# Performance work log

Measured on AMD Instinct MI355X. Metric: run time of the kernel, lower is better.

## Reference

```python
import jax, jax.numpy as jnp
import numpy as np

B, L, D, H = 2, 1024, 1024, 16
HEAD = D // H
BUCKETS = 256
MAX_REL = 512
ATT_SPAN = BUCKETS          # pos_ebd_size = position_buckets when buckets > 0
SCALE_FACTOR = 3            # 1 (content) + 1 (c2p) + 1 (p2c)


def _log_bucket(rel, bucket_size, max_position):
    """make_log_bucket_position: signed log-bucketed relative positions."""
    sign = jnp.sign(rel).astype(jnp.float32)
    mid = bucket_size // 2
    abs_pos = jnp.where((rel < mid) & (rel > -mid), mid - 1, jnp.abs(rel)).astype(jnp.float32)
    log_pos = jnp.ceil(jnp.log(abs_pos / mid) / np.float32(np.log((max_position - 1) / mid)) * (mid - 1)) + mid
    bucket = jnp.where(abs_pos <= mid, rel.astype(jnp.float32), log_pos * sign)
    return bucket.astype(jnp.int32)


def build_relative_position(q_len, k_len):
    rel = jnp.arange(q_len, dtype=jnp.int32)[:, None] - jnp.arange(k_len, dtype=jnp.int32)[None, :]
    return _log_bucket(rel, BUCKETS, MAX_REL)  # [q_len, k_len]


def setup_inputs() -> dict:
    key = jax.random.key(0)
    ks = jax.random.split(key, 6)
    w = 0.02  # typical init scale, keeps softmax well-conditioned
    return {
        "hidden_states": jax.random.normal(ks[0], (B, L, D), jnp.float32),
        "attention_mask": jnp.ones((B, L), jnp.int32),
        "rel_embeddings": jax.random.normal(ks[1], (2 * ATT_SPAN, D), jnp.float32) * w,
        "Wq": jax.random.normal(ks[2], (D, D), jnp.float32) * w,
        "bq": jnp.zeros((D,), jnp.float32),
        "Wk": jax.random.normal(ks[3], (D, D), jnp.float32) * w,
        "bk": jnp.zeros((D,), jnp.float32),
        "Wv": jax.random.normal(ks[4], (D, D), jnp.float32) * w,
        "bv": jnp.zeros((D,), jnp.float32),
    }


def reference(hidden_states, attention_mask, rel_embeddings, Wq, bq, Wk, bk, Wv, bv):
    Bn, Ln, Dn = hidden_states.shape

    def proj(x, W, b):  # Linear with bias, torch convention y = x W^T + b
        return x @ W.T + b

    def to_heads(x):  # [.., L, D] -> [.., H, L, HEAD]
        return x.reshape(*x.shape[:-1], H, HEAD).swapaxes(-3, -2)

    q = to_heads(proj(hidden_states, Wq, bq))  # [B,H,L,d]
    k = to_heads(proj(hidden_states, Wk, bk))
    v = to_heads(proj(hidden_states, Wv, bv))

    scale = jnp.sqrt(jnp.float32(HEAD * SCALE_FACTOR))
    scores = jnp.einsum('bhqd,bhkd->bhqk', q, k) / scale

    # disentangled relative-position bias (share_att_key=True -> reuse Wq/Wk)
    rel = build_relative_position(Ln, Ln)                     # [L,L] log-bucketed
    pos_k = proj(rel_embeddings, Wk, bk).reshape(2 * ATT_SPAN, H, HEAD)
    pos_q = proj(rel_embeddings, Wq, bq).reshape(2 * ATT_SPAN, H, HEAD)

    # c2p: Q . posK, gathered at (rel + span)
    c2p_att = jnp.einsum('bhqd,phd->bhqp', q, pos_k)          # [B,H,L,2S]
    c2p_idx = jnp.clip(rel + ATT_SPAN, 0, 2 * ATT_SPAN - 1)   # [L,L]
    c2p = jnp.take_along_axis(c2p_att, jnp.broadcast_to(c2p_idx[None, None], (Bn, H, Ln, Ln)), axis=-1)

    # p2c: K . posQ gathered at (-rel + span), then transposed to [q,k]
    p2c_att = jnp.einsum('bhkd,phd->bhkp', k, pos_q)          # [B,H,L,2S]
    p2c_idx = jnp.clip(-rel + ATT_SPAN, 0, 2 * ATT_SPAN - 1)
    p2c = jnp.take_along_axis(p2c_att, jnp.broadcast_to(p2c_idx[None, None], (Bn, H, Ln, Ln)), axis=-1)
    p2c = jnp.swapaxes(p2c, -1, -2)

    scores = scores + (c2p + p2c) / scale

    bias = jnp.where(attention_mask[:, None, None, :] > 0, 0.0, -1e9).astype(scores.dtype)
    probs = jax.nn.softmax(scores + bias, axis=-1)
    ctx = jnp.einsum('bhqk,bhkd->bhqd', probs, v)
    return ctx.swapaxes(1, 2).reshape(Bn, Ln, Dn)
```

## Files before the change

kernel.cpp:

```cpp
#include <hip/hip_runtime.h>


typedef short s8v __attribute__((ext_vector_type(8)));
typedef short s4v __attribute__((ext_vector_type(4)));
typedef float f32x4 __attribute__((ext_vector_type(4)));
typedef float f4v __attribute__((ext_vector_type(4)));

#define QK_SCALE 0.26864243f

__device__ __forceinline__ unsigned short f2bf(float f) {
  unsigned u = __builtin_bit_cast(unsigned, f);
  u += 0x7fffu + ((u >> 16) & 1u);
  return (unsigned short)(u >> 16);
}
__device__ __forceinline__ float bf2f(unsigned short h) {
  unsigned u = ((unsigned)h) << 16;
  return __builtin_bit_cast(float, u);
}

__device__ __forceinline__ void gload_lds16(const void* g, void* l) {
  __builtin_amdgcn_global_load_lds(
      (const __attribute__((address_space(1))) void*)g,
      (__attribute__((address_space(3))) void*)l, 16, 0, 0);
}

__global__ __launch_bounds__(256) void prep_kernel(
    const float* __restrict__ hidden, const float* __restrict__ rel,
    const float* __restrict__ Wq, const float* __restrict__ Wk,
    const float* __restrict__ Wv, const int* __restrict__ mask,
    short* __restrict__ Abf, short* __restrict__ Wbf,
    float* __restrict__ mbias, short* __restrict__ Tt) {
  int idx = blockIdx.x * 256 + threadIdx.x;
  const int NCONV = 1441792;
  if (idx < NCONV) {
    const float* src; short* dst; int off;
    if (idx < 524288) { src = hidden; dst = Abf; off = idx; }
    else if (idx < 655360) { src = rel; dst = Abf + 2048 * 1024; off = idx - 524288; }
    else {
      int j = idx - 655360;
      int w = j / 262144; off = j - w * 262144;
      src = (w == 0) ? Wq : (w == 1) ? Wk : Wv;
      dst = Wbf + w * 1048576;
    }
    f4v v = ((const f4v*)src)[off];
    s4v o;
    o[0] = (short)f2bf(v[0]); o[1] = (short)f2bf(v[1]);
    o[2] = (short)f2bf(v[2]); o[3] = (short)f2bf(v[3]);
    ((s4v*)dst)[off] = o;
  } else {
    int j = idx - NCONV;
    if (j < 2047) {
      int r = j - 1023;
      float fr = (float)r;
      float sign = (r > 0) ? 1.f : ((r < 0) ? -1.f : 0.f);
      float abs_pos = (r < 128 && r > -128) ? 127.f : fabsf(fr);
      const float logc = 1.3843393245589053f;
      float log_pos = ceilf(logf(abs_pos * (1.f / 128.f)) / logc * 127.f) + 128.f;
      float bucket = (abs_pos <= 128.f) ? fr : log_pos * sign;
      int bi = (int)bucket + 256;
      bi = bi < 0 ? 0 : (bi > 511 ? 511 : bi);
      Tt[j] = (short)bi;
    } else if (j < 4095) {
      int m = j - 2047;
      mbias[m] = (mask[m] > 0) ? 0.f : -1e9f;
    }
  }
}

__global__ __launch_bounds__(256) void gemm_qkv(
    const short* __restrict__ Abf, const short* __restrict__ Wbf,
    const float* __restrict__ bq, const float* __restrict__ bk,
    const float* __restrict__ bv,
    short* __restrict__ Qc, short* __restrict__ Kc, short* __restrict__ Vc) {
  __shared__ short As[128 * 64];
  __shared__ short Bs[128 * 64];
  int tid = threadIdx.x;
  int wid = tid >> 6, lane = tid & 63;
  int lr = lane & 15, lg = lane >> 4;
  int wr = wid >> 1, wc = wid & 1;
  int z = blockIdx.z;
  int brow = blockIdx.y * 128;
  if (z == 2 && brow >= 2048) return;
  const short* W = Wbf + z * 1048576;
  const float* bias = (z == 0) ? bq : (z == 1) ? bk : bv;
  short* C = (z == 0) ? Qc : (z == 1) ? Kc : Vc;
  float scale = (z == 2) ? 1.f : QK_SCALE;
  int bcol = blockIdx.x * 128;

  f32x4 acc[4][4];
  for (int i = 0; i < 4; i++)
    for (int j = 0; j < 4; j++) acc[i][j] = (f32x4){0.f, 0.f, 0.f, 0.f};

  for (int k0 = 0; k0 < 1024; k0 += 64) {
    for (int i = 0; i < 4; i++) {
      int n = i * 256 + wid * 64 + lane;
      const short* gA = Abf + (size_t)(brow + (n >> 3)) * 1024 + k0 + (n & 7) * 8;
      gload_lds16(gA, &As[(i * 256 + wid * 64) * 8]);
      const short* gB = W + (size_t)(bcol + (n >> 3)) * 1024 + k0 + (n & 7) * 8;
      gload_lds16(gB, &Bs[(i * 256 + wid * 64) * 8]);
    }
    __syncthreads();
    for (int ks = 0; ks < 2; ks++) {
      s8v af[4], bfv[4];
      for (int mi = 0; mi < 4; mi++)
        af[mi] = *(const s8v*)&As[(wr * 64 + mi * 16 + lr) * 64 + ks * 32 + lg * 8];
      for (int ni = 0; ni < 4; ni++)
        bfv[ni] = *(const s8v*)&Bs[(wc * 64 + ni * 16 + lr) * 64 + ks * 32 + lg * 8];
      for (int mi = 0; mi < 4; mi++)
        for (int ni = 0; ni < 4; ni++)
          acc[mi][ni] = __builtin_amdgcn_mfma_f32_16x16x32_bf16(
              af[mi], bfv[ni], acc[mi][ni], 0, 0, 0);
    }
    __syncthreads();
  }
  for (int mi = 0; mi < 4; mi++)
    for (int ni = 0; ni < 4; ni++) {
      int col = bcol + wc * 64 + ni * 16 + lr;
      float bb = bias[col];
      for (int r = 0; r < 4; r++) {
        int row = brow + wr * 64 + mi * 16 + lg * 4 + r;
        float v = (acc[mi][ni][r] + bb) * scale;
        C[(size_t)row * 1024 + col] = (short)f2bf(v);
      }
    }
}

__global__ __launch_bounds__(256) void pos_gemm(
    const short* __restrict__ Qc, const short* __restrict__ Kc,
    const float* __restrict__ mbias,
    short* __restrict__ c2p, short* __restrict__ p2c) {
  __shared__ short As[128 * 64];
  __shared__ short Bs[128 * 64];
  int tid = threadIdx.x;
  int wid = tid >> 6, lane = tid & 63;
  int lr = lane & 15, lg = lane >> 4;
  int wr = wid >> 1, wc = wid & 1;
  int zz = blockIdx.z;
  int which = zz >> 5;
  int bh = zz & 31;
  int b = bh >> 4, h = bh & 15;
  const short* Arows = (which == 0) ? Qc : Kc;
  const short* Brows = (which == 0) ? Kc : Qc;
  short* Out = (which == 0) ? c2p : p2c;
  int mrow = blockIdx.y * 128;
  int ncol = blockIdx.x * 128;

  for (int i = 0; i < 4; i++) {
    int n = i * 256 + wid * 64 + lane;
    const short* gA = Arows + (size_t)(b * 1024 + mrow + (n >> 3)) * 1024 + h * 64 + (n & 7) * 8;
    gload_lds16(gA, &As[(i * 256 + wid * 64) * 8]);
    const short* gB = Brows + (size_t)(2048 + ncol + (n >> 3)) * 1024 + h * 64 + (n & 7) * 8;
    gload_lds16(gB, &Bs[(i * 256 + wid * 64) * 8]);
  }
  __syncthreads();

  f32x4 acc[4][4];
  for (int i = 0; i < 4; i++)
    for (int j = 0; j < 4; j++) acc[i][j] = (f32x4){0.f, 0.f, 0.f, 0.f};
  for (int ks = 0; ks < 2; ks++) {
    s8v af[4], bfv[4];
    for (int mi = 0; mi < 4; mi++)
      af[mi] = *(const s8v*)&As[(wr * 64 + mi * 16 + lr) * 64 + ks * 32 + lg * 8];
    for (int ni = 0; ni < 4; ni++)
      bfv[ni] = *(const s8v*)&Bs[(wc * 64 + ni * 16 + lr) * 64 + ks * 32 + lg * 8];
    for (int mi = 0; mi < 4; mi++)
      for (int ni = 0; ni < 4; ni++)
        acc[mi][ni] = __builtin_amdgcn_mfma_f32_16x16x32_bf16(
            af[mi], bfv[ni], acc[mi][ni], 0, 0, 0);
  }
  size_t base = (size_t)(b * 16 + h) * 1024;
  for (int mi = 0; mi < 4; mi++)
    for (int ni = 0; ni < 4; ni++)
      for (int r = 0; r < 4; r++) {
        int m = mrow + wr * 64 + mi * 16 + lg * 4 + r;
        int nn = ncol + wc * 64 + ni * 16 + lr;
        float v = acc[mi][ni][r];
        if (which == 1) v += mbias[b * 1024 + m];
        Out[(base + m) * 512 + nn] = (short)f2bf(v);
      }
}

__global__ __launch_bounds__(256) void transpose_v(
    const short* __restrict__ Vc, short* __restrict__ Vt) {
  __shared__ short TL[64 * 72];
  int tid = threadIdx.x;
  int lt = blockIdx.x, h = blockIdx.y, b = blockIdx.z;
  for (int i = 0; i < 2; i++) {
    int n = i * 256 + tid;
    int l = n >> 3, c = n & 7;
    s8v v = *(const s8v*)&Vc[(size_t)(b * 1024 + lt * 64 + l) * 1024 + h * 64 + c * 8];
    *(s8v*)&TL[l * 72 + c * 8] = v;
  }
  __syncthreads();
  for (int i = 0; i < 2; i++) {
    int m = i * 256 + tid;
    int d = m >> 3, c = m & 7;
    s8v o;
    for (int jj = 0; jj < 8; jj++) o[jj] = TL[(c * 8 + jj) * 72 + d];
    *(s8v*)&Vt[((size_t)(b * 16 + h) * 64 + d) * 1024 + lt * 64 + c * 8] = o;
  }
}

template <int NSPLIT>
__global__ __launch_bounds__(256) void attn_kernel(
    const short* __restrict__ Qc, const short* __restrict__ Kc,
    const short* __restrict__ Vt, const short* __restrict__ c2p,
    const short* __restrict__ p2c, const short* __restrict__ Tt,
    float* __restrict__ Opart, float* __restrict__ dpart,
    float* __restrict__ out) {
  const int KSEG = 1024 / NSPLIT;
  const int NT = KSEG / 64;
  const int TLN = 64 + KSEG - 1;
  __shared__ short Kl[2][64 * 64];
  __shared__ short Vl[2][64 * 64];
  __shared__ short Pl[4][16 * 72];
  __shared__ short Tl[TLN + 1];
  int tid = threadIdx.x;
  int wid = tid >> 6, lane = tid & 63;
  int lr = lane & 15, lg = lane >> 4;
  int qt = blockIdx.x, h = blockIdx.y, z = blockIdx.z;
  int b = (NSPLIT == 1) ? z : (z >> 2);
  int ks = (NSPLIT == 1) ? 0 : (z & 3);
  int k0seg = ks * KSEG;
  int q0 = qt * 64, qbase = q0 + wid * 16;
  size_t bh1024 = (size_t)(b * 16 + h) * 1024;

  for (int i = tid; i < TLN; i += 256) Tl[i] = Tt[(q0 - k0seg - (KSEG - 1) + 1023) + i];

  s8v aq[2];
  for (int s_ = 0; s_ < 2; s_++)
    aq[s_] = *(const s8v*)&Qc[(size_t)(b * 1024 + qbase + lr) * 1024 + h * 64 + s_ * 32 + lg * 8];

  f32x4 oacc[4];
  for (int n = 0; n < 4; n++) oacc[n] = (f32x4){0.f, 0.f, 0.f, 0.f};
  float dsum[4] = {0.f, 0.f, 0.f, 0.f};
  __syncthreads();

  auto stage = [&](int t, int buf) {
#pragma unroll
    for (int i = 0; i < 2; i++) {
      int n = i * 256 + tid;
      int row = n >> 3, cswz = n & 7, cb = cswz ^ (row & 7);
      gload_lds16(&Kc[(size_t)(b * 1024 + k0seg + t * 64 + row) * 1024 + h * 64 + cb * 8],
                  &Kl[buf][(i * 256 + wid * 64) * 8]);
      gload_lds16(&Vt[((size_t)(b * 16 + h) * 64 + row) * 1024 + k0seg + t * 64 + cb * 8],
                  &Vl[buf][(i * 256 + wid * 64) * 8]);
    }
  };
  auto gather = [&](int t, unsigned short* cg, unsigned short* pg) {
#pragma unroll
    for (int n = 0; n < 4; n++) {
      int k = k0seg + t * 64 + n * 16 + lr;
      size_t prow = (bh1024 + k) * 512;
      int jb = wid * 16 - t * 64 - lr + (KSEG - 1) - n * 16 + lg * 4;
#pragma unroll
      for (int r = 0; r < 4; r++) {
        int q = qbase + lg * 4 + r;
        int idx = Tl[jb + r];
        cg[n * 4 + r] = (unsigned short)c2p[(bh1024 + q) * 512 + idx];
        pg[n * 4 + r] = (unsigned short)p2c[prow + idx];
      }
    }
  };

  unsigned short c2g[16], p2g[16], c2n[16], p2n[16];
  stage(0, 0);
  gather(0, c2g, p2g);
  __syncthreads();

#pragma unroll
  for (int t = 0; t < NT; ++t) {
    const int cur = t & 1, nxt = cur ^ 1;

    if (t + 1 < NT) {
      stage(t + 1, nxt);
      gather(t + 1, c2n, p2n);
    }

    f32x4 sacc[4];
#pragma unroll
    for (int n = 0; n < 4; n++) sacc[n] = (f32x4){0.f, 0.f, 0.f, 0.f};
#pragma unroll
    for (int s_ = 0; s_ < 2; s_++)
#pragma unroll
      for (int n = 0; n < 4; n++) {
        int row = n * 16 + lr, cb = s_ * 4 + lg, cbs = cb ^ (row & 7);
        s8v bk_ = *(const s8v*)&Kl[cur][row * 64 + cbs * 8];
        sacc[n] = __builtin_amdgcn_mfma_f32_16x16x32_bf16(aq[s_], bk_, sacc[n], 0, 0, 0);
      }

#pragma unroll
    for (int n = 0; n < 4; n++)
#pragma unroll
      for (int r = 0; r < 4; r++) {
        float bias = bf2f(c2g[n * 4 + r]) + bf2f(p2g[n * 4 + r]);
        float p = __expf(sacc[n][r] + bias);
        dsum[r] += p;
        Pl[wid][(lg * 4 + r) * 72 + n * 16 + lr] = (short)f2bf(p);
      }
    asm volatile("s_waitcnt lgkmcnt(0)" ::: "memory");

#pragma unroll
    for (int s_ = 0; s_ < 2; s_++) {
      s8v ap = *(const s8v*)&Pl[wid][lr * 72 + s_ * 32 + lg * 8];
#pragma unroll
      for (int n = 0; n < 4; n++) {
        int row = n * 16 + lr, cb = s_ * 4 + lg, cbs = cb ^ (row & 7);
        s8v bv_ = *(const s8v*)&Vl[cur][row * 64 + cbs * 8];
        oacc[n] = __builtin_amdgcn_mfma_f32_16x16x32_bf16(ap, bv_, oacc[n], 0, 0, 0);
      }
    }

    __syncthreads();

    if (t + 1 < NT) {
#pragma unroll
      for (int i = 0; i < 16; i++) { c2g[i] = c2n[i]; p2g[i] = p2n[i]; }
    }
  }

  for (int m = 1; m < 16; m <<= 1)
    for (int r = 0; r < 4; r++) dsum[r] += __shfl_xor(dsum[r], m, 64);

  if (NSPLIT == 1) {
    for (int n = 0; n < 4; n++)
      for (int r = 0; r < 4; r++) {
        int q = qbase + lg * 4 + r;
        int d = n * 16 + lr;
        out[(size_t)(b * 1024 + q) * 1024 + h * 64 + d] = oacc[n][r] / dsum[r];
      }
  } else {
    size_t po = ((size_t)(z * 16 + h)) * 65536;
    for (int n = 0; n < 4; n++)
      for (int r = 0; r < 4; r++) {
        int q = qbase + lg * 4 + r;
        Opart[po + (size_t)q * 64 + n * 16 + lr] = oacc[n][r];
      }
    if (lr == 0)
      for (int r = 0; r < 4; r++)
        dpart[(z * 16 + h) * 1024 + qbase + lg * 4 + r] = dsum[r];
  }
}

__global__ __launch_bounds__(256) void combine_kernel(
    const float* __restrict__ Opart, const float* __restrict__ dpart,
    float* __restrict__ out) {
  int idx = blockIdx.x * 256 + threadIdx.x;
  int pos = idx * 4;
  int b = pos >> 20;
  int q = (pos >> 10) & 1023;
  int hd = pos & 1023;
  int h = hd >> 6, d = hd & 63;
  f4v s = (f4v){0.f, 0.f, 0.f, 0.f};
  float dn = 0.f;
  for (int ks = 0; ks < 4; ks++) {
    int zh = (b * 4 + ks) * 16 + h;
    s += *(const f4v*)&Opart[(size_t)zh * 65536 + q * 64 + d];
    dn += dpart[zh * 1024 + q];
  }
  f4v r = s / dn;
  *(f4v*)&out[pos] = r;
}

extern "C" void kernel_launch(void* const* d_in, const int* in_sizes, int n_in,
                              void* d_out, int out_size, void* d_ws, size_t ws_size,
                              hipStream_t stream) {
  (void)in_sizes; (void)n_in; (void)out_size;
  const float* hidden = (const float*)d_in[0];
  const int* mask = (const int*)d_in[1];
  const float* rel = (const float*)d_in[2];
  const float* Wq = (const float*)d_in[3];
  const float* bq = (const float*)d_in[4];
  const float* Wk = (const float*)d_in[5];
  const float* bk = (const float*)d_in[6];
  const float* Wv = (const float*)d_in[7];
  const float* bv = (const float*)d_in[8];
  float* out = (float*)d_out;

  char* w = (char*)d_ws;
  short* Abf = (short*)w; w += 2560 * 1024 * 2;
  short* Wbf = (short*)w; w += 3 * 1024 * 1024 * 2;
  short* Qc  = (short*)w; w += 2560 * 1024 * 2;
  short* Kc  = (short*)w; w += 2560 * 1024 * 2;
  short* Vc  = (short*)w; w += 2560 * 1024 * 2;
  short* Vt  = (short*)w; w += 2 * 16 * 64 * 1024 * 2;
  short* c2p = (short*)w; w += (size_t)2 * 16 * 1024 * 512 * 2;
  short* p2c = (short*)w; w += (size_t)2 * 16 * 1024 * 512 * 2;
  short* Tt  = (short*)w; w += 4096;
  float* mbias = (float*)w; w += 8192;
  float* Opart = (float*)w; w += (size_t)8 * 16 * 1024 * 64 * 4;
  float* dpart = (float*)w; w += 8 * 16 * 1024 * 4;
  size_t need = (size_t)(w - (char*)d_ws);

  prep_kernel<<<5648, 256, 0, stream>>>(hidden, rel, Wq, Wk, Wv, mask, Abf, Wbf, mbias, Tt);
  gemm_qkv<<<dim3(8, 20, 3), 256, 0, stream>>>(Abf, Wbf, bq, bk, bv, Qc, Kc, Vc);
  pos_gemm<<<dim3(4, 8, 64), 256, 0, stream>>>(Qc, Kc, mbias, c2p, p2c);
  transpose_v<<<dim3(16, 16, 2), 256, 0, stream>>>(Vc, Vt);
  if (ws_size >= need) {
    attn_kernel<4><<<dim3(16, 16, 8), 256, 0, stream>>>(Qc, Kc, Vt, c2p, p2c, Tt,
                                                        Opart, dpart, out);
    combine_kernel<<<2048, 256, 0, stream>>>(Opart, dpart, out);
  } else {
    attn_kernel<1><<<dim3(16, 16, 2), 256, 0, stream>>>(Qc, Kc, Vt, c2p, p2c, Tt,
                                                        Opart, dpart, out);
  }
}
```

Before: 155.6 us.

## Precompute relative-position bias into MFMA-fragment layout before attention

Adds a bias_build kernel that gathers c2p and p2c through LDS windows, sums them, and writes a bf16 bias tensor pre-arranged in the attention kernel's MFMA fragment order. The attention kernel then reads two coalesced 16-byte vectors per tile instead of doing 32 scattered 2-byte gathers from c2p/p2c. Opart and dpart now reuse the c2p/p2c buffers, which are dead after bias_build, so the workspace fits. The cost is an extra kernel launch plus writing and reading a full B*H*L*L bf16 bias tensor (about 64 MB).

Result: faster. 149.5 us (-3.9%).

```diff
diff --git a/kernel.cpp b/kernel.cpp
--- a/kernel.cpp
+++ b/kernel.cpp
@@ -201,8 +201,184 @@
   }
 }
 
+__global__ __launch_bounds__(256) void bias_build(
+    const short* __restrict__ c2p, const short* __restrict__ p2c,
+    const short* __restrict__ Tt, short* __restrict__ bias) {
+  __shared__ short Wc[64 * 66];
+  __shared__ short Wp[64 * 66];
+  __shared__ short Tl[128];
+  int tid = threadIdx.x;
+  int wid = tid >> 6, lane = tid & 63;
+  int lr = lane & 15, lg = lane >> 4;
+  int qt = blockIdx.x, kt = blockIdx.y, bh = blockIdx.z;
+  int q0 = qt * 64, k0 = kt * 64;
+  int relbase = q0 - k0;
+  size_t bh1024 = (size_t)bh * 1024;
+
+  if (tid < 127) Tl[tid] = Tt[relbase + 960 + tid];
+  __syncthreads();
+
+#pragma unroll
+  for (int ii = 0; ii < 16; ii++) {
+    int row = wid * 16 + ii;
+    int w0 = Tl[row];
+    int col = w0 + lane; col = col > 511 ? 511 : col;
+    Wc[row * 66 + lane] = c2p[(bh1024 + q0 + row) * 512 + col];
+    int w0p_ = Tl[63 - row];
+    int colp = w0p_ + lane; colp = colp > 511 ? 511 : colp;
+    Wp[row * 66 + lane] = p2c[(bh1024 + k0 + row) * 512 + colp];
+  }
+  __syncthreads();
+
+  int w0c[4], w0p[4];
+#pragma unroll
+  for (int r = 0; r < 4; r++) w0c[r] = Tl[wid * 16 + lg * 4 + r];
+#pragma unroll
+  for (int n = 0; n < 4; n++) w0p[n] = Tl[63 - (n * 16 + lr)];
+
+  s8v o0, o1;
+#pragma unroll
+  for (int n = 0; n < 4; n++)
+#pragma unroll
+    for (int r = 0; r < 4; r++) {
+      int qq = wid * 16 + lg * 4 + r;
+      int kk = n * 16 + lr;
+      int p = Tl[qq - kk + 63];
+      float v = bf2f((unsigned short)Wc[qq * 66 + p - w0c[r]]) +
+                bf2f((unsigned short)Wp[kk * 66 + p - w0p[n]]);
+      short s = (short)f2bf(v);
+      if (n < 2) o0[(n & 1) * 4 + r] = s; else o1[(n & 1) * 4 + r] = s;
+    }
+  size_t tile = ((size_t)bh * 16 + qt) * 16 + kt;
+  size_t base = (tile * 4 + wid) * 1024 + lane * 8;
+  *(s8v*)&bias[base] = o0;
+  *(s8v*)&bias[base + 512] = o1;
+}
+
 template <int NSPLIT>
-__global__ __launch_bounds__(256) void attn_kernel(
+__global__ __launch_bounds__(256) void attn_frag(
+    const short* __restrict__ Qc, const short* __restrict__ Kc,
+    const short* __restrict__ Vt, const short* __restrict__ bias,
+    float* __restrict__ Opart, float* __restrict__ dpart,
+    float* __restrict__ out) {
+  const int KSEG = 1024 / NSPLIT;
+  const int NT = KSEG / 64;
+  __shared__ short Kl[2][64 * 64];
+  __shared__ short Vl[2][64 * 64];
+  __shared__ short Pl[4][16 * 72];
+  int tid = threadIdx.x;
+  int wid = tid >> 6, lane = tid & 63;
+  int lr = lane & 15, lg = lane >> 4;
+  int qt = blockIdx.x, h = blockIdx.y, z = blockIdx.z;
+  int b = (NSPLIT == 1) ? z : (z >> 2);
+  int ks = (NSPLIT == 1) ? 0 : (z & 3);
+  int k0seg = ks * KSEG;
+  int q0 = qt * 64, qbase = q0 + wid * 16;
+
+  s8v aq[2];
+  for (int s_ = 0; s_ < 2; s_++)
+    aq[s_] = *(const s8v*)&Qc[(size_t)(b * 1024 + qbase + lr) * 1024 + h * 64 + s_ * 32 + lg * 8];
+
+  f32x4 oacc[4];
+  for (int n = 0; n < 4; n++) oacc[n] = (f32x4){0.f, 0.f, 0.f, 0.f};
+  float dsum[4] = {0.f, 0.f, 0.f, 0.f};
+
+  auto stage = [&](int t, int buf) {
+#pragma unroll
+    for (int i = 0; i < 2; i++) {
+      int n = i * 256 + tid;
+      int row = n >> 3, cswz = n & 7, cb = cswz ^ (row & 7);
+      gload_lds16(&Kc[(size_t)(b * 1024 + k0seg + t * 64 + row) * 1024 + h * 64 + cb * 8],
+                  &Kl[buf][(i * 256 + wid * 64) * 8]);
+      gload_lds16(&Vt[((size_t)(b * 16 + h) * 64 + row) * 1024 + k0seg + t * 64 + cb * 8],
+                  &Vl[buf][(i * 256 + wid * 64) * 8]);
+    }
+  };
+  auto fload = [&](int t, s8v& f0, s8v& f1) {
+    size_t tile = (((size_t)(b * 16 + h) * 16 + qt) * 16 + (k0seg >> 6) + t);
+    size_t base = (tile * 4 + wid) * 1024 + lane * 8;
+    f0 = *(const s8v*)&bias[base];
+    f1 = *(const s8v*)&bias[base + 512];
+  };
+
+  s8v fb0, fb1, fn0, fn1;
+  stage(0, 0);
+  fload(0, fb0, fb1);
+  __syncthreads();
+
+#pragma unroll
+  for (int t = 0; t < NT; ++t) {
+    const int cur = t & 1, nxt = cur ^ 1;
+
+    if (t + 1 < NT) {
+      stage(t + 1, nxt);
+      fload(t + 1, fn0, fn1);
+    }
+
+    f32x4 sacc[4];
+#pragma unroll
+    for (int n = 0; n < 4; n++) sacc[n] = (f32x4){0.f, 0.f, 0.f, 0.f};
+#pragma unroll
+    for (int s_ = 0; s_ < 2; s_++)
+#pragma unroll
+      for (int n = 0; n < 4; n++) {
+        int row = n * 16 + lr, cb = s_ * 4 + lg, cbs = cb ^ (row & 7);
+        s8v bk_ = *(const s8v*)&Kl[cur][row * 64 + cbs * 8];
+        sacc[n] = __builtin_amdgcn_mfma_f32_16x16x32_bf16(aq[s_], bk_, sacc[n], 0, 0, 0);
+      }
+
+#pragma unroll
+    for (int n = 0; n < 4; n++)
+#pragma unroll
+      for (int r = 0; r < 4; r++) {
+        unsigned short bv_ = (unsigned short)((n < 2 ? fb0 : fb1)[(n & 1) * 4 + r]);
+        float p = __expf(sacc[n][r] + bf2f(bv_));
+        dsum[r] += p;
+        Pl[wid][(lg * 4 + r) * 72 + n * 16 + lr] = (short)f2bf(p);
+      }
+    asm volatile("s_waitcnt lgkmcnt(0)" ::: "memory");
+
+#pragma unroll
+    for (int s_ = 0; s_ < 2; s_++) {
+      s8v ap = *(const s8v*)&Pl[wid][lr * 72 + s_ * 32 + lg * 8];
+#pragma unroll
+      for (int n = 0; n < 4; n++) {
+        int row = n * 16 + lr, cb = s_ * 4 + lg, cbs = cb ^ (row & 7);
+        s8v bv_ = *(const s8v*)&Vl[cur][row * 64 + cbs * 8];
+        oacc[n] = __builtin_amdgcn_mfma_f32_16x16x32_bf16(ap, bv_, oacc[n], 0, 0, 0);
+      }
+    }
+
+    __syncthreads();
+
+    if (t + 1 < NT) { fb0 = fn0; fb1 = fn1; }
+  }
+
+  for (int m = 1; m < 16; m <<= 1)
+    for (int r = 0; r < 4; r++) dsum[r] += __shfl_xor(dsum[r], m, 64);
+
+  if (NSPLIT == 1) {
+    for (int n = 0; n < 4; n++)
+      for (int r = 0; r < 4; r++) {
+        int q = qbase + lg * 4 + r;
+        int d = n * 16 + lr;
+        out[(size_t)(b * 1024 + q) * 1024 + h * 64 + d] = oacc[n][r] / dsum[r];
+      }
+  } else {
+    size_t po = ((size_t)(z * 16 + h)) * 65536;
+    for (int n = 0; n < 4; n++)
+      for (int r = 0; r < 4; r++) {
+        int q = qbase + lg * 4 + r;
+        Opart[po + (size_t)q * 64 + n * 16 + lr] = oacc[n][r];
+      }
+    if (lr == 0)
+      for (int r = 0; r < 4; r++)
+        dpart[(z * 16 + h) * 1024 + qbase + lg * 4 + r] = dsum[r];
+  }
+}
+
+template <int NSPLIT>
+__global__ __launch_bounds__(256) void attn_gather(
     const short* __restrict__ Qc, const short* __restrict__ Kc,
     const short* __restrict__ Vt, const short* __restrict__ c2p,
     const short* __restrict__ p2c, const short* __restrict__ Tt,
@@ -271,11 +447,7 @@
 #pragma unroll
   for (int t = 0; t < NT; ++t) {
     const int cur = t & 1, nxt = cur ^ 1;
-
-    if (t + 1 < NT) {
-      stage(t + 1, nxt);
-      gather(t + 1, c2n, p2n);
-    }
+    if (t + 1 < NT) { stage(t + 1, nxt); gather(t + 1, c2n, p2n); }
 
     f32x4 sacc[4];
 #pragma unroll
@@ -288,7 +460,6 @@
         s8v bk_ = *(const s8v*)&Kl[cur][row * 64 + cbs * 8];
         sacc[n] = __builtin_amdgcn_mfma_f32_16x16x32_bf16(aq[s_], bk_, sacc[n], 0, 0, 0);
       }
-
 #pragma unroll
     for (int n = 0; n < 4; n++)
 #pragma unroll
@@ -299,7 +470,6 @@
         Pl[wid][(lg * 4 + r) * 72 + n * 16 + lr] = (short)f2bf(p);
       }
     asm volatile("s_waitcnt lgkmcnt(0)" ::: "memory");
-
 #pragma unroll
     for (int s_ = 0; s_ < 2; s_++) {
       s8v ap = *(const s8v*)&Pl[wid][lr * 72 + s_ * 32 + lg * 8];
@@ -310,9 +480,7 @@
         oacc[n] = __builtin_amdgcn_mfma_f32_16x16x32_bf16(ap, bv_, oacc[n], 0, 0, 0);
       }
     }
-
     __syncthreads();
-
     if (t + 1 < NT) {
 #pragma unroll
       for (int i = 0; i < 16; i++) { c2g[i] = c2n[i]; p2g[i] = p2n[i]; }
@@ -388,20 +556,31 @@
   short* p2c = (short*)w; w += (size_t)2 * 16 * 1024 * 512 * 2;
   short* Tt  = (short*)w; w += 4096;
   float* mbias = (float*)w; w += 8192;
-  float* Opart = (float*)w; w += (size_t)8 * 16 * 1024 * 64 * 4;
-  float* dpart = (float*)w; w += 8 * 16 * 1024 * 4;
-  size_t need = (size_t)(w - (char*)d_ws);
+  short* bias_frag = (short*)w;
+  size_t need_frag = (size_t)(w - (char*)d_ws) + (size_t)8192 * 4096 * 2;
+  float* Opart_old = (float*)w;
+  size_t need_old = (size_t)(w - (char*)d_ws) + (size_t)8 * 16 * 1024 * 64 * 4 + 8 * 16 * 1024 * 4;
 
   prep_kernel<<<5648, 256, 0, stream>>>(hidden, rel, Wq, Wk, Wv, mask, Abf, Wbf, mbias, Tt);
   gemm_qkv<<<dim3(8, 20, 3), 256, 0, stream>>>(Abf, Wbf, bq, bk, bv, Qc, Kc, Vc);
   pos_gemm<<<dim3(4, 8, 64), 256, 0, stream>>>(Qc, Kc, mbias, c2p, p2c);
   transpose_v<<<dim3(16, 16, 2), 256, 0, stream>>>(Vc, Vt);
-  if (ws_size >= need) {
-    attn_kernel<4><<<dim3(16, 16, 8), 256, 0, stream>>>(Qc, Kc, Vt, c2p, p2c, Tt,
+
+  if (ws_size >= need_frag) {
+    float* Opart = (float*)c2p;
+    float* dpart = (float*)p2c;
+    bias_build<<<dim3(16, 16, 32), 256, 0, stream>>>(c2p, p2c, Tt, bias_frag);
+    attn_frag<4><<<dim3(16, 16, 8), 256, 0, stream>>>(Qc, Kc, Vt, bias_frag,
+                                                      Opart, dpart, out);
+    combine_kernel<<<2048, 256, 0, stream>>>(Opart, dpart, out);
+  } else if (ws_size >= need_old) {
+    float* Opart = Opart_old;
+    float* dpart = (float*)((char*)Opart_old + (size_t)8 * 16 * 1024 * 64 * 4);
+    attn_gather<4><<<dim3(16, 16, 8), 256, 0, stream>>>(Qc, Kc, Vt, c2p, p2c, Tt,
                                                         Opart, dpart, out);
     combine_kernel<<<2048, 256, 0, stream>>>(Opart, dpart, out);
   } else {
-    attn_kernel<1><<<dim3(16, 16, 2), 256, 0, stream>>>(Qc, Kc, Vt, c2p, p2c, Tt,
-                                                        Opart, dpart, out);
-  }
-}
+    attn_gather<1><<<dim3(16, 16, 2), 256, 0, stream>>>(Qc, Kc, Vt, c2p, p2c, Tt,
+                                                        (float*)Opart_old, (float*)Opart_old, out);
+  }
+}
```
